# Kernel tuning notes

Hardware: AMD Instinct MI355X
Metric: run time of the kernel (lower is better)

Reference implementation:

```python
import jax, jax.numpy as jnp
import numpy as np

B, N, M = 1024, 1024, 64


def setup_inputs() -> dict:
    key = jax.random.key(0)
    ks = jax.random.split(key, 9)
    return {
        "memory": jax.random.normal(ks[0], (B, N, M), dtype=jnp.float32),
        "k": jax.random.normal(ks[1], (B, M), dtype=jnp.float32),
        "beta": jax.random.uniform(ks[2], (B, 1), dtype=jnp.float32),
        "g": jax.random.uniform(ks[3], (B, 1), dtype=jnp.float32),
        "s": jax.random.uniform(ks[4], (B, 3), dtype=jnp.float32),
        "gamma": jax.random.uniform(ks[5], (B, 1), dtype=jnp.float32),
        "w_prev": jax.random.uniform(ks[6], (B, N), dtype=jnp.float32),
        "e": jax.random.uniform(ks[7], (B, M), dtype=jnp.float32),
        "a": jax.random.normal(ks[8], (B, M), dtype=jnp.float32),
    }


def reference(memory, k, beta, g, s, gamma, w_prev, e, a):
    EPS = 1e-16
    COS_EPS = 1e-8  # torch cosine_similarity norm clamp

    # --- _similarity: content addressing (cosine sim + softmax over N) ---
    mem_e = memory + EPS                      # (B, N, M)
    k_e = (k + EPS)[:, None, :]               # (B, 1, M)
    dot = jnp.sum(mem_e * k_e, axis=-1)       # (B, N)
    denom = (jnp.maximum(jnp.linalg.norm(mem_e, axis=-1), COS_EPS)
             * jnp.maximum(jnp.linalg.norm(k_e, axis=-1), COS_EPS))
    wc = jax.nn.softmax(beta * (dot / denom), axis=1)  # (B, N)

    # --- _interpolate ---
    wg = g * wc + (1.0 - g) * w_prev           # (B, N)

    # --- _shift: 3-tap circular convolution, vectorized over batch ---
    # c[i] = s[0]*w[i-1] + s[1]*w[i] + s[2]*w[i+1]  (circular)
    w_hat = (s[:, 0:1] * jnp.roll(wg, 1, axis=1)
             + s[:, 1:2] * wg
             + s[:, 2:3] * jnp.roll(wg, -1, axis=1))

    # --- _sharpen ---
    w = w_hat ** gamma
    w = w / (jnp.sum(w, axis=1, keepdims=True) + EPS)  # (B, N)

    # --- read ---
    read = jnp.einsum('bn,bnm->bm', w, memory)         # (B, M)

    # --- write: rank-1 erase / add ---
    erase = w[:, :, None] * e[:, None, :]              # (B, N, M)
    add = w[:, :, None] * a[:, None, :]                # (B, N, M)
    new_mem = memory * (1.0 - erase) + add             # (B, N, M)

    # pack read (as an extra row) with the updated memory: (B, N+1, M)
    return jnp.concatenate([read[:, None, :], new_mem], axis=1)
```

## Files before the change

### kernel.cpp

```cpp
#include <hip/hip_runtime.h>
#include <cmath>

#define NB   1024
#define NN   1024
#define MM   64
#define NT   512
#define NW   (NT / 64)
#define ITS  (NN / 32)
#define GRID 256
#define BPB  (NB / GRID)

typedef float f32x4 __attribute__((ext_vector_type(4)));

__device__ __forceinline__ float block_sum(float v, float* s_tmp) {
    #pragma unroll
    for (int off = 32; off > 0; off >>= 1) v += __shfl_xor(v, off, 64);
    if ((threadIdx.x & 63) == 0) s_tmp[threadIdx.x >> 6] = v;
    __syncthreads();
    float r = 0.0f;
    #pragma unroll
    for (int i = 0; i < NW; ++i) r += s_tmp[i];
    __syncthreads();
    return r;
}

__device__ __forceinline__ float block_max(float v, float* s_tmp) {
    #pragma unroll
    for (int off = 32; off > 0; off >>= 1) v = fmaxf(v, __shfl_xor(v, off, 64));
    if ((threadIdx.x & 63) == 0) s_tmp[threadIdx.x >> 6] = v;
    __syncthreads();
    float r = s_tmp[0];
    #pragma unroll
    for (int i = 1; i < NW; ++i) r = fmaxf(r, s_tmp[i]);
    __syncthreads();
    return r;
}

template<bool PF>
__device__ __forceinline__ void process_batch(
    int b,
    f32x4 (&mc)[ITS],
    const float* __restrict__ memory,
    const float* __restrict__ k,
    const float* __restrict__ beta,
    const float* __restrict__ g,
    const float* __restrict__ s,
    const float* __restrict__ gamma,
    const float* __restrict__ w_prev,
    const float* __restrict__ e,
    const float* __restrict__ a,
    float* __restrict__ out,
    float* s_sc, float* s_w, float* s_k, float* s_tmp, f32x4* s_red)
{
    const int t    = threadIdx.x;
    const int cg   = t & 15;
    const int rg   = t >> 4;
    const int wid  = t >> 6;
    const int lane = t & 63;
    const int coff = 4 * cg;

    const float* membn = memory + (size_t)(b + 1) * NN * MM;
    float*       outb  = out    + (size_t)b * (NN + 1) * MM;

    const float bet = beta[b], gb = g[b];
    const float s0 = s[b * 3 + 0], s1 = s[b * 3 + 1], s2 = s[b * 3 + 2];
    const float gam = gamma[b];
    const float wp0 = w_prev[(size_t)b * NN + t];
    const float wp1 = w_prev[(size_t)b * NN + t + 512];
    const f32x4 e4 = *(const f32x4*)(e + b * MM + coff);
    const f32x4 a4 = *(const f32x4*)(a + b * MM + coff);

    if (t < MM) s_k[t] = k[b * MM + t] + 1e-16f;
    float kq = (t < MM) ? s_k[t] * s_k[t] : 0.0f;
    float kden = fmaxf(sqrtf(block_sum(kq, s_tmp)), 1e-8f);
    const f32x4 k4 = ((const f32x4*)s_k)[cg];

    #pragma unroll
    for (int it = 0; it < ITS; ++it) {
        int n = it * 32 + rg;
        f32x4 m4 = mc[it];
        float ex = m4.x + 1e-16f, ey = m4.y + 1e-16f;
        float ez = m4.z + 1e-16f, ew = m4.w + 1e-16f;
        float d = ex * k4.x + ey * k4.y + ez * k4.z + ew * k4.w;
        float q = ex * ex + ey * ey + ez * ez + ew * ew;
        #pragma unroll
        for (int off = 8; off > 0; off >>= 1) {
            d += __shfl_xor(d, off, 64);
            q += __shfl_xor(q, off, 64);
        }
        if (cg == 0) s_sc[n] = bet * d / (fmaxf(sqrtf(q), 1e-8f) * kden);
    }
    __syncthreads();

    float sc0 = s_sc[t], sc1 = s_sc[t + 512];
    float mx = block_max(fmaxf(sc0, sc1), s_tmp);
    float e0 = __expf(sc0 - mx), e1 = __expf(sc1 - mx);
    float inv = 1.0f / block_sum(e0 + e1, s_tmp);

    const float omg = 1.0f - gb;
    s_sc[t]       = gb * e0 * inv + omg * wp0;
    s_sc[t + 512] = gb * e1 * inv + omg * wp1;
    __syncthreads();

    float wv0, wv1;
    {
        int nm = (t == 0) ? NN - 1 : t - 1;
        wv0 = powf(s0 * s_sc[nm] + s1 * s_sc[t] + s2 * s_sc[t + 1], gam);
    }
    {
        int n = t + 512;
        int np = (n == NN - 1) ? 0 : n + 1;
        wv1 = powf(s0 * s_sc[n - 1] + s1 * s_sc[n] + s2 * s_sc[np], gam);
    }
    float winv = 1.0f / (block_sum(wv0 + wv1, s_tmp) + 1e-16f);
    s_w[t]       = wv0 * winv;
    s_w[t + 512] = wv1 * winv;
    __syncthreads();

    f32x4 acc = {0.f, 0.f, 0.f, 0.f};
    #pragma unroll
    for (int it = 0; it < ITS; ++it) {
        int n = it * 32 + rg;
        f32x4 m4 = mc[it];
        float wn = s_w[n];
        acc.x += wn * m4.x; acc.y += wn * m4.y;
        acc.z += wn * m4.z; acc.w += wn * m4.w;
        f32x4 o;
        o.x = m4.x * (1.0f - wn * e4.x) + wn * a4.x;
        o.y = m4.y * (1.0f - wn * e4.y) + wn * a4.y;
        o.z = m4.z * (1.0f - wn * e4.z) + wn * a4.z;
        o.w = m4.w * (1.0f - wn * e4.w) + wn * a4.w;
        __builtin_nontemporal_store(o, (f32x4*)(outb + (size_t)(n + 1) * MM + coff));
        if constexpr (PF) {
            mc[it] = __builtin_nontemporal_load(
                (const f32x4*)(membn + (size_t)n * MM + coff));
        }
    }

    #pragma unroll
    for (int off = 16; off <= 32; off <<= 1) {
        acc.x += __shfl_xor(acc.x, off, 64);
        acc.y += __shfl_xor(acc.y, off, 64);
        acc.z += __shfl_xor(acc.z, off, 64);
        acc.w += __shfl_xor(acc.w, off, 64);
    }
    if (lane < 16) s_red[wid * 16 + lane] = acc;
    __syncthreads();
    if (t < 16) {
        f32x4 r = {0.f, 0.f, 0.f, 0.f};
        #pragma unroll
        for (int wv = 0; wv < NW; ++wv) {
            f32x4 v = s_red[wv * 16 + t];
            r.x += v.x; r.y += v.y; r.z += v.z; r.w += v.w;
        }
        __builtin_nontemporal_store(r, (f32x4*)(outb + 4 * t));
    }
    __syncthreads();
}

__global__ void __launch_bounds__(NT, 2) ntm_fused(
    const float* __restrict__ memory,
    const float* __restrict__ k,
    const float* __restrict__ beta,
    const float* __restrict__ g,
    const float* __restrict__ s,
    const float* __restrict__ gamma,
    const float* __restrict__ w_prev,
    const float* __restrict__ e,
    const float* __restrict__ a,
    float* __restrict__ out)
{
    __shared__ float  s_sc[NN];
    __shared__ float  s_w[NN];
    __shared__ float  s_k[MM];
    __shared__ float  s_tmp[NW];
    __shared__ f32x4  s_red[NW * 16];

    const int t    = threadIdx.x;
    const int cg   = t & 15;
    const int rg   = t >> 4;
    const int coff = 4 * cg;

    f32x4 mc[ITS];
    const int bbase = blockIdx.x * BPB;

    {
        const float* memb = memory + (size_t)bbase * NN * MM;
        #pragma unroll
        for (int it = 0; it < ITS; ++it)
            mc[it] = __builtin_nontemporal_load(
                (const f32x4*)(memb + (size_t)(it * 32 + rg) * MM + coff));
    }

    for (int bi = 0; bi < BPB - 1; ++bi)
        process_batch<true>(bbase + bi, mc, memory, k, beta, g, s, gamma,
                            w_prev, e, a, out, s_sc, s_w, s_k, s_tmp, s_red);
    process_batch<false>(bbase + BPB - 1, mc, memory, k, beta, g, s, gamma,
                         w_prev, e, a, out, s_sc, s_w, s_k, s_tmp, s_red);
}

extern "C" void kernel_launch(void* const* d_in, const int* in_sizes, int n_in,
                              void* d_out, int out_size, void* d_ws, size_t ws_size,
                              hipStream_t stream) {
    ntm_fused<<<GRID, NT, 0, stream>>>(
        (const float*)d_in[0],
        (const float*)d_in[1],
        (const float*)d_in[2],
        (const float*)d_in[3],
        (const float*)d_in[4],
        (const float*)d_in[5],
        (const float*)d_in[6],
        (const float*)d_in[7],
        (const float*)d_in[8],
        (float*)d_out);
}
```

Before: 498.1 us.

## Prefetch per-batch operands and replace syncthreads with LDS-only barriers

Per-batch small operands (k, beta, g, s, gamma, w_prev, e, a) are loaded one batch ahead into a register struct. The key norm is computed with a 16-lane shuffle instead of a block-wide reduction, which removes the shared-memory key buffer and two barriers. Every __syncthreads is replaced by an inline-asm barrier that waits only on LDS counters, so outstanding global prefetch loads of memory are not drained at each barrier. The cost is extra registers held live across the batch loop, and correctness now depends on the barrier not needing to wait for vmem operations.

```diff
diff --git a/kernel.cpp b/kernel.cpp
--- a/kernel.cpp
+++ b/kernel.cpp
@@ -12,15 +12,19 @@
 
 typedef float f32x4 __attribute__((ext_vector_type(4)));
 
+__device__ __forceinline__ void lds_barrier() {
+    asm volatile("s_waitcnt lgkmcnt(0)\n\ts_barrier" ::: "memory");
+}
+
 __device__ __forceinline__ float block_sum(float v, float* s_tmp) {
     #pragma unroll
     for (int off = 32; off > 0; off >>= 1) v += __shfl_xor(v, off, 64);
     if ((threadIdx.x & 63) == 0) s_tmp[threadIdx.x >> 6] = v;
-    __syncthreads();
+    lds_barrier();
     float r = 0.0f;
     #pragma unroll
     for (int i = 0; i < NW; ++i) r += s_tmp[i];
-    __syncthreads();
+    lds_barrier();
     return r;
 }
 
@@ -28,18 +32,49 @@
     #pragma unroll
     for (int off = 32; off > 0; off >>= 1) v = fmaxf(v, __shfl_xor(v, off, 64));
     if ((threadIdx.x & 63) == 0) s_tmp[threadIdx.x >> 6] = v;
-    __syncthreads();
+    lds_barrier();
     float r = s_tmp[0];
     #pragma unroll
     for (int i = 1; i < NW; ++i) r = fmaxf(r, s_tmp[i]);
-    __syncthreads();
+    lds_barrier();
     return r;
 }
 
+struct Ops {
+    f32x4 k4, e4, a4;
+    float kden, bet, gb, s0, s1, s2, gam, wp0, wp1;
+};
+
+__device__ __forceinline__ Ops load_ops(
+    int b, int coff,
+    const float* __restrict__ k, const float* __restrict__ beta,
+    const float* __restrict__ g, const float* __restrict__ s,
+    const float* __restrict__ gamma, const float* __restrict__ w_prev,
+    const float* __restrict__ e, const float* __restrict__ a)
+{
+    Ops o;
+    const int t = threadIdx.x;
+    f32x4 kv = *(const f32x4*)(k + b * MM + coff);
+    o.k4.x = kv.x + 1e-16f; o.k4.y = kv.y + 1e-16f;
+    o.k4.z = kv.z + 1e-16f; o.k4.w = kv.w + 1e-16f;
+    float kq = o.k4.x * o.k4.x + o.k4.y * o.k4.y
+             + o.k4.z * o.k4.z + o.k4.w * o.k4.w;
+    #pragma unroll
+    for (int off = 8; off > 0; off >>= 1) kq += __shfl_xor(kq, off, 64);
+    o.kden = fmaxf(sqrtf(kq), 1e-8f);
+    o.e4 = *(const f32x4*)(e + b * MM + coff);
+    o.a4 = *(const f32x4*)(a + b * MM + coff);
+    o.bet = beta[b]; o.gb = g[b];
+    o.s0 = s[b * 3 + 0]; o.s1 = s[b * 3 + 1]; o.s2 = s[b * 3 + 2];
+    o.gam = gamma[b];
+    o.wp0 = w_prev[(size_t)b * NN + t];
+    o.wp1 = w_prev[(size_t)b * NN + t + 512];
+    return o;
+}
+
 template<bool PF>
-__device__ __forceinline__ void process_batch(
-    int b,
-    f32x4 (&mc)[ITS],
+__device__ __forceinline__ Ops process_batch(
+    int b, f32x4 (&mc)[ITS], Ops op,
     const float* __restrict__ memory,
     const float* __restrict__ k,
     const float* __restrict__ beta,
@@ -50,7 +85,7 @@
     const float* __restrict__ e,
     const float* __restrict__ a,
     float* __restrict__ out,
-    float* s_sc, float* s_w, float* s_k, float* s_tmp, f32x4* s_red)
+    float* s_sc, float* s_w, float* s_tmp, f32x4* s_red)
 {
     const int t    = threadIdx.x;
     const int cg   = t & 15;
@@ -62,60 +97,51 @@
     const float* membn = memory + (size_t)(b + 1) * NN * MM;
     float*       outb  = out    + (size_t)b * (NN + 1) * MM;
 
-    const float bet = beta[b], gb = g[b];
-    const float s0 = s[b * 3 + 0], s1 = s[b * 3 + 1], s2 = s[b * 3 + 2];
-    const float gam = gamma[b];
-    const float wp0 = w_prev[(size_t)b * NN + t];
-    const float wp1 = w_prev[(size_t)b * NN + t + 512];
-    const f32x4 e4 = *(const f32x4*)(e + b * MM + coff);
-    const f32x4 a4 = *(const f32x4*)(a + b * MM + coff);
-
-    if (t < MM) s_k[t] = k[b * MM + t] + 1e-16f;
-    float kq = (t < MM) ? s_k[t] * s_k[t] : 0.0f;
-    float kden = fmaxf(sqrtf(block_sum(kq, s_tmp)), 1e-8f);
-    const f32x4 k4 = ((const f32x4*)s_k)[cg];
-
     #pragma unroll
     for (int it = 0; it < ITS; ++it) {
         int n = it * 32 + rg;
         f32x4 m4 = mc[it];
         float ex = m4.x + 1e-16f, ey = m4.y + 1e-16f;
         float ez = m4.z + 1e-16f, ew = m4.w + 1e-16f;
-        float d = ex * k4.x + ey * k4.y + ez * k4.z + ew * k4.w;
+        float d = ex * op.k4.x + ey * op.k4.y + ez * op.k4.z + ew * op.k4.w;
         float q = ex * ex + ey * ey + ez * ez + ew * ew;
         #pragma unroll
         for (int off = 8; off > 0; off >>= 1) {
             d += __shfl_xor(d, off, 64);
             q += __shfl_xor(q, off, 64);
         }
-        if (cg == 0) s_sc[n] = bet * d / (fmaxf(sqrtf(q), 1e-8f) * kden);
-    }
-    __syncthreads();
+        if (cg == 0) s_sc[n] = op.bet * d / (fmaxf(sqrtf(q), 1e-8f) * op.kden);
+    }
+    lds_barrier();
+
+    Ops opn = op;
+    if constexpr (PF)
+        opn = load_ops(b + 1, coff, k, beta, g, s, gamma, w_prev, e, a);
 
     float sc0 = s_sc[t], sc1 = s_sc[t + 512];
     float mx = block_max(fmaxf(sc0, sc1), s_tmp);
     float e0 = __expf(sc0 - mx), e1 = __expf(sc1 - mx);
     float inv = 1.0f / block_sum(e0 + e1, s_tmp);
 
-    const float omg = 1.0f - gb;
-    s_sc[t]       = gb * e0 * inv + omg * wp0;
-    s_sc[t + 512] = gb * e1 * inv + omg * wp1;
-    __syncthreads();
+    const float omg = 1.0f - op.gb;
+    s_sc[t]       = op.gb * e0 * inv + omg * op.wp0;
+    s_sc[t + 512] = op.gb * e1 * inv + omg * op.wp1;
+    lds_barrier();
 
     float wv0, wv1;
     {
         int nm = (t == 0) ? NN - 1 : t - 1;
-        wv0 = powf(s0 * s_sc[nm] + s1 * s_sc[t] + s2 * s_sc[t + 1], gam);
+        wv0 = powf(op.s0 * s_sc[nm] + op.s1 * s_sc[t] + op.s2 * s_sc[t + 1], op.gam);
     }
     {
         int n = t + 512;
         int np = (n == NN - 1) ? 0 : n + 1;
-        wv1 = powf(s0 * s_sc[n - 1] + s1 * s_sc[n] + s2 * s_sc[np], gam);
+        wv1 = powf(op.s0 * s_sc[n - 1] + op.s1 * s_sc[n] + op.s2 * s_sc[np], op.gam);
     }
     float winv = 1.0f / (block_sum(wv0 + wv1, s_tmp) + 1e-16f);
     s_w[t]       = wv0 * winv;
     s_w[t + 512] = wv1 * winv;
-    __syncthreads();
+    lds_barrier();
 
     f32x4 acc = {0.f, 0.f, 0.f, 0.f};
     #pragma unroll
@@ -126,10 +152,10 @@
         acc.x += wn * m4.x; acc.y += wn * m4.y;
         acc.z += wn * m4.z; acc.w += wn * m4.w;
         f32x4 o;
-        o.x = m4.x * (1.0f - wn * e4.x) + wn * a4.x;
-        o.y = m4.y * (1.0f - wn * e4.y) + wn * a4.y;
-        o.z = m4.z * (1.0f - wn * e4.z) + wn * a4.z;
-        o.w = m4.w * (1.0f - wn * e4.w) + wn * a4.w;
+        o.x = m4.x * (1.0f - wn * op.e4.x) + wn * op.a4.x;
+        o.y = m4.y * (1.0f - wn * op.e4.y) + wn * op.a4.y;
+        o.z = m4.z * (1.0f - wn * op.e4.z) + wn * op.a4.z;
+        o.w = m4.w * (1.0f - wn * op.e4.w) + wn * op.a4.w;
         __builtin_nontemporal_store(o, (f32x4*)(outb + (size_t)(n + 1) * MM + coff));
         if constexpr (PF) {
             mc[it] = __builtin_nontemporal_load(
@@ -145,7 +171,7 @@
         acc.w += __shfl_xor(acc.w, off, 64);
     }
     if (lane < 16) s_red[wid * 16 + lane] = acc;
-    __syncthreads();
+    lds_barrier();
     if (t < 16) {
         f32x4 r = {0.f, 0.f, 0.f, 0.f};
         #pragma unroll
@@ -155,7 +181,8 @@
         }
         __builtin_nontemporal_store(r, (f32x4*)(outb + 4 * t));
     }
-    __syncthreads();
+    lds_barrier();
+    return opn;
 }
 
 __global__ void __launch_bounds__(NT, 2) ntm_fused(
@@ -172,7 +199,6 @@
 {
     __shared__ float  s_sc[NN];
     __shared__ float  s_w[NN];
-    __shared__ float  s_k[MM];
     __shared__ float  s_tmp[NW];
     __shared__ f32x4  s_red[NW * 16];
 
@@ -184,6 +210,7 @@
     f32x4 mc[ITS];
     const int bbase = blockIdx.x * BPB;
 
+    Ops op = load_ops(bbase, coff, k, beta, g, s, gamma, w_prev, e, a);
     {
         const float* memb = memory + (size_t)bbase * NN * MM;
         #pragma unroll
@@ -193,10 +220,12 @@
     }
 
     for (int bi = 0; bi < BPB - 1; ++bi)
-        process_batch<true>(bbase + bi, mc, memory, k, beta, g, s, gamma,
-                            w_prev, e, a, out, s_sc, s_w, s_k, s_tmp, s_red);
-    process_batch<false>(bbase + BPB - 1, mc, memory, k, beta, g, s, gamma,
-                         w_prev, e, a, out, s_sc, s_w, s_k, s_tmp, s_red);
+        op = process_batch<true>(bbase + bi, mc, op, memory, k, beta, g, s,
+                                 gamma, w_prev, e, a, out,
+                                 s_sc, s_w, s_tmp, s_red);
+    process_batch<false>(bbase + BPB - 1, mc, op, memory, k, beta, g, s,
+                         gamma, w_prev, e, a, out,
+                         s_sc, s_w, s_tmp, s_red);
 }
 
 extern "C" void kernel_launch(void* const* d_in, const int* in_sizes, int n_in,
```

Measured after the change: 470.8 us. 5.5% less time.
